# Optimization experiments

Measured on AMD Instinct MI355X. Metric: run time of the kernel, lower is better.

The kernel has to match this reference:

```python
import jax, jax.numpy as jnp
import numpy as np

NUM_HEADS = 16
HEAD_DIM = 128
MODEL_DIM = 2048
SEQ = 4096
INIT = 0.02


def setup_inputs() -> dict:
    key = jax.random.key(0)
    k1, k2, k3 = jax.random.split(key, 3)
    x = jax.random.normal(k1, (SEQ, MODEL_DIM), dtype=jnp.float32)
    w_attn = jax.random.normal(k2, (MODEL_DIM, 3 * MODEL_DIM), dtype=jnp.float32) * INIT
    b_attn = jnp.zeros((3 * MODEL_DIM,), dtype=jnp.float32)
    w_proj = jax.random.normal(k3, (MODEL_DIM, MODEL_DIM), dtype=jnp.float32) * INIT
    b_proj = jnp.zeros((MODEL_DIM,), dtype=jnp.float32)
    return {"x": x, "w_attn": w_attn, "b_attn": b_attn, "w_proj": w_proj, "b_proj": b_proj}


def reference(x, w_attn, b_attn, w_proj, b_proj):
    seq = x.shape[0]
    # fused QKV projection: [seq, 3*model_dim]
    hidden = x @ w_attn + b_attn
    q, k, v = jnp.split(hidden, 3, axis=-1)
    q = q.reshape(seq, NUM_HEADS, HEAD_DIM)
    k = k.reshape(seq, NUM_HEADS, HEAD_DIM)
    v = v.reshape(seq, NUM_HEADS, HEAD_DIM)
    q = q / jnp.sqrt(jnp.asarray(HEAD_DIM, dtype=q.dtype))
    # scores: [heads, q, k]
    scores = jnp.einsum('qhd,khd->hqk', q, k)
    causal = jnp.tril(jnp.ones((seq, seq), dtype=bool))  # mask[q, k]
    big_neg = jnp.finfo(jnp.float32).min
    scores = jnp.where(causal[None, :, :], scores, big_neg)
    pattern = jax.nn.softmax(scores, axis=-1)
    z = jnp.einsum('hqk,khd->qhd', pattern, v)
    out = z.reshape(seq, MODEL_DIM) @ w_proj + b_proj
    return out
```

## Files before the change

### kernel.cpp

```cpp
#include <hip/hip_runtime.h>
#include <hip/hip_bf16.h>
#include <stdint.h>
#include <stddef.h>

typedef __bf16 bf16_8 __attribute__((ext_vector_type(8)));
typedef __bf16 bf16_4 __attribute__((ext_vector_type(4)));
typedef float f32x4 __attribute__((ext_vector_type(4)));

#define BIG_NEG (-1e30f)
#define QSCALE (0.08838834764831845f * 1.4426950408889634f)
#define FIXMAX 16.0f

__device__ __forceinline__ void gld_lds16(const void* g, void* l) {
  __builtin_amdgcn_global_load_lds(
      (const __attribute__((address_space(1))) uint32_t*)g,
      (__attribute__((address_space(3))) uint32_t*)l, 16, 0, 0);
}

__global__ __launch_bounds__(256) void convert_bf16(
    const float* __restrict__ in, __bf16* __restrict__ out, long long n) {
  long long i = ((long long)blockIdx.x * 256 + threadIdx.x) * 8;
  if (i + 8 > n) return;
  const float4* in4 = (const float4*)(in + i);
  float4 a = in4[0], b = in4[1];
  bf16_8 o = {(__bf16)a.x, (__bf16)a.y, (__bf16)a.z, (__bf16)a.w,
              (__bf16)b.x, (__bf16)b.y, (__bf16)b.z, (__bf16)b.w};
  *(bf16_8*)(out + i) = o;
}

__global__ __launch_bounds__(256) void transpose_cvt(
    const float* __restrict__ in, __bf16* __restrict__ out, int R, int C) {
  __shared__ __bf16 tile[32][33];
  int bx = blockIdx.x * 32;
  int by = blockIdx.y * 32;
  int tx = threadIdx.x;
  int ty = threadIdx.y;
#pragma unroll
  for (int j = 0; j < 32; j += 8)
    tile[ty + j][tx] = (__bf16)in[(size_t)(by + ty + j) * C + bx + tx];
  __syncthreads();
#pragma unroll
  for (int j = 0; j < 32; j += 8)
    out[(size_t)(bx + ty + j) * R + by + tx] = tile[tx][ty + j];
}

__global__ __launch_bounds__(256) void gemm_bt(
    const __bf16* __restrict__ A, const __bf16* __restrict__ Bt,
    const float* __restrict__ bias, __bf16* __restrict__ C0,
    __bf16* __restrict__ VT, float* __restrict__ Cf,
    int M, int N, int K, int mode) {
  __shared__ __bf16 As[128 * 32];
  __shared__ __bf16 Bs[128 * 32];

  const int t = threadIdx.x;
  const int lane = t & 63;
  const int wave = t >> 6;
  const int col = lane & 15;
  const int quad = lane >> 4;
  const int wm = (wave >> 1) * 64;
  const int wn = (wave & 1) * 64;
  const int m0 = blockIdx.y * 128;
  const int n0 = blockIdx.x * 128;
  const bool vswap = (mode == 1) && (n0 >= 4096);

  const int srow = t >> 2;
  const int scol = (t & 3) * 8;
  const __bf16* ga0 = A + (size_t)(m0 + srow) * K + scol;
  const __bf16* ga1 = ga0 + (size_t)64 * K;
  const __bf16* gb0 = Bt + (size_t)(n0 + srow) * K + scol;
  const __bf16* gb1 = gb0 + (size_t)64 * K;
  __bf16* lA0 = As + wave * 512;
  __bf16* lA1 = As + 2048 + wave * 512;
  __bf16* lB0 = Bs + wave * 512;
  __bf16* lB1 = Bs + 2048 + wave * 512;

  f32x4 acc[4][4];
#pragma unroll
  for (int i = 0; i < 4; i++)
#pragma unroll
    for (int j = 0; j < 4; j++) acc[i][j] = f32x4{0.f, 0.f, 0.f, 0.f};

  for (int k0 = 0; k0 < K; k0 += 32) {
    __syncthreads();
    gld_lds16(ga0 + k0, lA0);
    gld_lds16(ga1 + k0, lA1);
    gld_lds16(gb0 + k0, lB0);
    gld_lds16(gb1 + k0, lB1);
    __syncthreads();

    bf16_8 af[4], bfr[4];
#pragma unroll
    for (int i = 0; i < 4; i++) {
      af[i] = *(const bf16_8*)(As + (wm + i * 16 + col) * 32 + quad * 8);
      bfr[i] = *(const bf16_8*)(Bs + (wn + i * 16 + col) * 32 + quad * 8);
    }
    if (!vswap) {
#pragma unroll
      for (int mi = 0; mi < 4; mi++)
#pragma unroll
        for (int ni = 0; ni < 4; ni++)
          acc[mi][ni] = __builtin_amdgcn_mfma_f32_16x16x32_bf16(
              af[mi], bfr[ni], acc[mi][ni], 0, 0, 0);
    } else {
#pragma unroll
      for (int mi = 0; mi < 4; mi++)
#pragma unroll
        for (int ni = 0; ni < 4; ni++)
          acc[mi][ni] = __builtin_amdgcn_mfma_f32_16x16x32_bf16(
              bfr[ni], af[mi], acc[mi][ni], 0, 0, 0);
    }
  }

  if (mode == 0) {
#pragma unroll
    for (int mi = 0; mi < 4; mi++)
#pragma unroll
      for (int ni = 0; ni < 4; ni++) {
        int gn = n0 + wn + ni * 16 + col;
        float bv = bias[gn];
#pragma unroll
        for (int r = 0; r < 4; r++)
          Cf[(size_t)(m0 + wm + mi * 16 + quad * 4 + r) * N + gn] =
              acc[mi][ni][r] + bv;
      }
  } else if (n0 < 2048) {
#pragma unroll
    for (int mi = 0; mi < 4; mi++)
#pragma unroll
      for (int ni = 0; ni < 4; ni++) {
        int gn = n0 + wn + ni * 16 + col;
        float bv = bias[gn];
#pragma unroll
        for (int r = 0; r < 4; r++)
          C0[(size_t)(m0 + wm + mi * 16 + quad * 4 + r) * 4096 + gn] =
              (__bf16)((acc[mi][ni][r] + bv) * QSCALE);
      }
  } else if (n0 < 4096) {
#pragma unroll
    for (int mi = 0; mi < 4; mi++)
#pragma unroll
      for (int ni = 0; ni < 4; ni++) {
        int gn = n0 + wn + ni * 16 + col;
        float bv = bias[gn];
#pragma unroll
        for (int r = 0; r < 4; r++)
          C0[(size_t)(m0 + wm + mi * 16 + quad * 4 + r) * 4096 + gn] =
              (__bf16)(acc[mi][ni][r] + bv);
      }
  } else {
#pragma unroll
    for (int mi = 0; mi < 4; mi++) {
      int seq = m0 + wm + mi * 16 + col;
#pragma unroll
      for (int ni = 0; ni < 4; ni++) {
#pragma unroll
        for (int r = 0; r < 4; r++) {
          int gn = n0 + wn + ni * 16 + quad * 4 + r;
          float bv = bias[gn];
          VT[(size_t)(gn - 4096) * M + seq] = (__bf16)(acc[mi][ni][r] + bv);
        }
      }
    }
  }
}

__global__ __launch_bounds__(256, 2) void flash_attn(
    const __bf16* __restrict__ QK, const __bf16* __restrict__ VT,
    __bf16* __restrict__ Z) {
  constexpr int KS = 136;
  constexpr int VS = 68;
  constexpr int PS = 72;
  __shared__ __bf16 Ks[64 * KS];
  __shared__ __bf16 Vs[128 * VS];
  __shared__ __bf16 Ps[2 * 4 * 16 * PS];

  const int t = threadIdx.x;
  const int lane = t & 63;
  const int wave = t >> 6;
  const int col = lane & 15;
  const int quad = lane >> 4;
  const int h = blockIdx.y;
  const int a = blockIdx.x;
  const int q0_lo = a * 64;
  const int q0_hi = (63 - a) * 64;
  const int nkb = 64 - a;

  const __bf16* kbase =
      QK + (size_t)(t >> 4) * 4096 + 2048 + h * 128 + (t & 15) * 8;
  __bf16* kdst = Ks + (t >> 4) * KS + (t & 15) * 8;
  const __bf16* vbase = VT + (size_t)(h * 128 + (t >> 3)) * 4096 + (t & 7) * 8;
  __bf16* vdst = Vs + (t >> 3) * VS + (t & 7) * 8;

  bf16_8 qf_hi[4], qf_lo[4];
  {
    const __bf16* qh = QK + (size_t)(q0_hi + wave * 16 + col) * 4096 + h * 128;
    const __bf16* ql = QK + (size_t)(q0_lo + wave * 16 + col) * 4096 + h * 128;
#pragma unroll
    for (int i = 0; i < 4; i++) {
      qf_hi[i] = *(const bf16_8*)(qh + i * 32 + quad * 8);
      qf_lo[i] = *(const bf16_8*)(ql + i * 32 + quad * 8);
    }
  }

  f32x4 z_hi[8], z_lo[8];
#pragma unroll
  for (int i = 0; i < 8; i++) {
    z_hi[i] = f32x4{0.f, 0.f, 0.f, 0.f};
    z_lo[i] = f32x4{0.f, 0.f, 0.f, 0.f};
  }
  float l_hi = 0.f, l_lo = 0.f;

  bf16_8 kpre[4], vpre[4];
#pragma unroll
  for (int j = 0; j < 4; j++) {
    kpre[j] = *(const bf16_8*)(kbase + (size_t)j * 16 * 4096);
    vpre[j] = *(const bf16_8*)(vbase + (size_t)j * 32 * 4096);
  }

  __bf16* pwh = Ps + wave * 16 * PS;
  __bf16* pwl = Ps + (4 + wave) * 16 * PS;

  for (int kb = 0; kb < nkb; kb++) {
    const int k0 = kb * 64;
    const bool lo_on = (kb <= a);
    __syncthreads();
#pragma unroll
    for (int j = 0; j < 4; j++) {
      *(bf16_8*)(kdst + j * 16 * KS) = kpre[j];
      *(bf16_8*)(vdst + j * 32 * VS) = vpre[j];
    }
    __syncthreads();

    if (kb + 1 < nkb) {
      const __bf16* kb2 = kbase + (size_t)(k0 + 64) * 4096;
      const __bf16* vb2 = vbase + (k0 + 64);
#pragma unroll
      for (int j = 0; j < 4; j++) {
        kpre[j] = *(const bf16_8*)(kb2 + (size_t)j * 16 * 4096);
        vpre[j] = *(const bf16_8*)(vb2 + (size_t)j * 32 * 4096);
      }
    }

    f32x4 sh[4], sl[4];
#pragma unroll
    for (int p = 0; p < 4; p++) {
      sh[p] = f32x4{0.f, 0.f, 0.f, 0.f};
      sl[p] = f32x4{0.f, 0.f, 0.f, 0.f};
#pragma unroll
      for (int kd = 0; kd < 4; kd++) {
        bf16_8 kf =
            *(const bf16_8*)(Ks + (p * 16 + col) * KS + kd * 32 + quad * 8);
        sh[p] =
            __builtin_amdgcn_mfma_f32_16x16x32_bf16(kf, qf_hi[kd], sh[p], 0, 0, 0);
        if (lo_on)
          sl[p] = __builtin_amdgcn_mfma_f32_16x16x32_bf16(kf, qf_lo[kd], sl[p],
                                                          0, 0, 0);
      }
    }

    if (kb == nkb - 1) {
      int qg = q0_hi + wave * 16 + col;
#pragma unroll
      for (int p = 0; p < 4; p++)
#pragma unroll
        for (int r = 0; r < 4; r++)
          if (k0 + p * 16 + quad * 4 + r > qg) sh[p][r] = BIG_NEG;
    }
    if (kb == a) {
      int qg = q0_lo + wave * 16 + col;
#pragma unroll
      for (int p = 0; p < 4; p++)
#pragma unroll
        for (int r = 0; r < 4; r++)
          if (k0 + p * 16 + quad * 4 + r > qg) sl[p][r] = BIG_NEG;
    }

    {
      float rs = 0.f;
#pragma unroll
      for (int p = 0; p < 4; p++) {
        float e0 = exp2f(sh[p][0] - FIXMAX);
        float e1 = exp2f(sh[p][1] - FIXMAX);
        float e2 = exp2f(sh[p][2] - FIXMAX);
        float e3 = exp2f(sh[p][3] - FIXMAX);
        rs += (e0 + e1) + (e2 + e3);
        bf16_4 pk = {(__bf16)e0, (__bf16)e1, (__bf16)e2, (__bf16)e3};
        *(bf16_4*)(pwh + col * PS + p * 16 + quad * 4) = pk;
      }
      l_hi += rs;
    }
    if (lo_on) {
      float rs = 0.f;
#pragma unroll
      for (int p = 0; p < 4; p++) {
        float e0 = exp2f(sl[p][0] - FIXMAX);
        float e1 = exp2f(sl[p][1] - FIXMAX);
        float e2 = exp2f(sl[p][2] - FIXMAX);
        float e3 = exp2f(sl[p][3] - FIXMAX);
        rs += (e0 + e1) + (e2 + e3);
        bf16_4 pk = {(__bf16)e0, (__bf16)e1, (__bf16)e2, (__bf16)e3};
        *(bf16_4*)(pwl + col * PS + p * 16 + quad * 4) = pk;
      }
      l_lo += rs;
    }

    bf16_8 ph0 = *(const bf16_8*)(pwh + col * PS + quad * 8);
    bf16_8 ph1 = *(const bf16_8*)(pwh + col * PS + 32 + quad * 8);
    bf16_8 pl0, pl1;
    if (lo_on) {
      pl0 = *(const bf16_8*)(pwl + col * PS + quad * 8);
      pl1 = *(const bf16_8*)(pwl + col * PS + 32 + quad * 8);
    }

#pragma unroll
    for (int db = 0; db < 8; db++) {
      bf16_8 vf0 = *(const bf16_8*)(Vs + (db * 16 + col) * VS + quad * 8);
      z_hi[db] =
          __builtin_amdgcn_mfma_f32_16x16x32_bf16(vf0, ph0, z_hi[db], 0, 0, 0);
      if (lo_on)
        z_lo[db] =
            __builtin_amdgcn_mfma_f32_16x16x32_bf16(vf0, pl0, z_lo[db], 0, 0, 0);
      bf16_8 vf1 = *(const bf16_8*)(Vs + (db * 16 + col) * VS + 32 + quad * 8);
      z_hi[db] =
          __builtin_amdgcn_mfma_f32_16x16x32_bf16(vf1, ph1, z_hi[db], 0, 0, 0);
      if (lo_on)
        z_lo[db] =
            __builtin_amdgcn_mfma_f32_16x16x32_bf16(vf1, pl1, z_lo[db], 0, 0, 0);
    }
  }

  {
    float l = l_hi;
    l += __shfl_xor(l, 16, 64);
    l += __shfl_xor(l, 32, 64);
    float rl = 1.f / l;
    __bf16* zrow =
        Z + (size_t)(q0_hi + wave * 16 + col) * 2048 + h * 128 + quad * 4;
#pragma unroll
    for (int db = 0; db < 8; db++) {
      bf16_4 o = {(__bf16)(z_hi[db][0] * rl), (__bf16)(z_hi[db][1] * rl),
                  (__bf16)(z_hi[db][2] * rl), (__bf16)(z_hi[db][3] * rl)};
      *(bf16_4*)(zrow + db * 16) = o;
    }
  }
  {
    float l = l_lo;
    l += __shfl_xor(l, 16, 64);
    l += __shfl_xor(l, 32, 64);
    float rl = 1.f / l;
    __bf16* zrow =
        Z + (size_t)(q0_lo + wave * 16 + col) * 2048 + h * 128 + quad * 4;
#pragma unroll
    for (int db = 0; db < 8; db++) {
      bf16_4 o = {(__bf16)(z_lo[db][0] * rl), (__bf16)(z_lo[db][1] * rl),
                  (__bf16)(z_lo[db][2] * rl), (__bf16)(z_lo[db][3] * rl)};
      *(bf16_4*)(zrow + db * 16) = o;
    }
  }
}

extern "C" void kernel_launch(void* const* d_in, const int* in_sizes, int n_in,
                              void* d_out, int out_size, void* d_ws,
                              size_t ws_size, hipStream_t stream) {
  const float* x = (const float*)d_in[0];
  const float* w_attn = (const float*)d_in[1];
  const float* b_attn = (const float*)d_in[2];
  const float* w_proj = (const float*)d_in[3];
  const float* b_proj = (const float*)d_in[4];
  float* out = (float*)d_out;

  __bf16* ws = (__bf16*)d_ws;
  __bf16* QK = ws;
  __bf16* VT = ws + 16777216;
  __bf16* WT1 = ws + 25165824;
  __bf16* Zb = ws + 25165824;
  __bf16* WT2 = ws + 37748736;
  __bf16* xb = ws + 41943040;

  convert_bf16<<<4096, 256, 0, stream>>>(x, xb, 8388608LL);
  transpose_cvt<<<dim3(6144 / 32, 2048 / 32), dim3(32, 8), 0, stream>>>(
      w_attn, WT1, 2048, 6144);
  transpose_cvt<<<dim3(2048 / 32, 2048 / 32), dim3(32, 8), 0, stream>>>(
      w_proj, WT2, 2048, 2048);

  gemm_bt<<<dim3(6144 / 128, 4096 / 128), 256, 0, stream>>>(
      xb, WT1, b_attn, QK, VT, nullptr, 4096, 6144, 2048, 1);

  flash_attn<<<dim3(32, 16), 256, 0, stream>>>(QK, VT, Zb);

  gemm_bt<<<dim3(2048 / 128, 4096 / 128), 256, 0, stream>>>(
      Zb, WT2, b_proj, nullptr, nullptr, out, 4096, 2048, 2048, 0);
}
```

Before: 576.5 us.

## Triple-buffer GEMM LDS tiles with async global-to-LDS prefetch

Replaces the single-buffered K loop of the bf16 GEMM with a three-stage LDS ring. Loads for tile kt+2 are issued before computing tile kt, and a partial vmcnt wait plus one barrier per iteration replaces the two syncthreads. This hides global load latency behind MFMA work. LDS use triples to 48KB per block, which can lower occupancy, and the hand-written waitcnt logic adds a risk of ordering errors.

```diff
diff --git a/kernel.cpp b/kernel.cpp
--- a/kernel.cpp
+++ b/kernel.cpp
@@ -49,8 +49,8 @@
     const float* __restrict__ bias, __bf16* __restrict__ C0,
     __bf16* __restrict__ VT, float* __restrict__ Cf,
     int M, int N, int K, int mode) {
-  __shared__ __bf16 As[128 * 32];
-  __shared__ __bf16 Bs[128 * 32];
+  __shared__ __bf16 As[3][128 * 32];
+  __shared__ __bf16 Bs[3][128 * 32];
 
   const int t = threadIdx.x;
   const int lane = t & 63;
@@ -69,10 +69,7 @@
   const __bf16* ga1 = ga0 + (size_t)64 * K;
   const __bf16* gb0 = Bt + (size_t)(n0 + srow) * K + scol;
   const __bf16* gb1 = gb0 + (size_t)64 * K;
-  __bf16* lA0 = As + wave * 512;
-  __bf16* lA1 = As + 2048 + wave * 512;
-  __bf16* lB0 = Bs + wave * 512;
-  __bf16* lB1 = Bs + 2048 + wave * 512;
+  const int ldo = wave * 512;
 
   f32x4 acc[4][4];
 #pragma unroll
@@ -80,19 +77,31 @@
 #pragma unroll
     for (int j = 0; j < 4; j++) acc[i][j] = f32x4{0.f, 0.f, 0.f, 0.f};
 
-  for (int k0 = 0; k0 < K; k0 += 32) {
-    __syncthreads();
-    gld_lds16(ga0 + k0, lA0);
-    gld_lds16(ga1 + k0, lA1);
-    gld_lds16(gb0 + k0, lB0);
-    gld_lds16(gb1 + k0, lB1);
-    __syncthreads();
+  const int nk = K / 32;
+
+#define STAGE(b, k0)                          \
+  do {                                        \
+    gld_lds16(ga0 + (k0), As[b] + ldo);       \
+    gld_lds16(ga1 + (k0), As[b] + 2048 + ldo);\
+    gld_lds16(gb0 + (k0), Bs[b] + ldo);       \
+    gld_lds16(gb1 + (k0), Bs[b] + 2048 + ldo);\
+  } while (0)
+
+  STAGE(0, 0);
+  STAGE(1, 32);
+  asm volatile("s_waitcnt vmcnt(4)" ::: "memory");
+  __builtin_amdgcn_s_barrier();
+  asm volatile("" ::: "memory");
+
+  for (int kt = 0; kt < nk; ++kt) {
+    const int b = kt % 3;
+    if (kt + 2 < nk) STAGE((kt + 2) % 3, (kt + 2) * 32);
 
     bf16_8 af[4], bfr[4];
 #pragma unroll
     for (int i = 0; i < 4; i++) {
-      af[i] = *(const bf16_8*)(As + (wm + i * 16 + col) * 32 + quad * 8);
-      bfr[i] = *(const bf16_8*)(Bs + (wn + i * 16 + col) * 32 + quad * 8);
+      af[i] = *(const bf16_8*)(As[b] + (wm + i * 16 + col) * 32 + quad * 8);
+      bfr[i] = *(const bf16_8*)(Bs[b] + (wn + i * 16 + col) * 32 + quad * 8);
     }
     if (!vswap) {
 #pragma unroll
@@ -109,7 +118,17 @@
           acc[mi][ni] = __builtin_amdgcn_mfma_f32_16x16x32_bf16(
               bfr[ni], af[mi], acc[mi][ni], 0, 0, 0);
     }
-  }
+
+    if (kt + 1 < nk) {
+      if (kt + 2 < nk)
+        asm volatile("s_waitcnt vmcnt(4)" ::: "memory");
+      else
+        asm volatile("s_waitcnt vmcnt(0)" ::: "memory");
+      __builtin_amdgcn_s_barrier();
+      asm volatile("" ::: "memory");
+    }
+  }
+#undef STAGE
 
   if (mode == 0) {
 #pragma unroll
```

New measurement: 584.3 us. No clear change (+1.4%).

## Rewrite GEMM as 256x256 tile, double-buffered, swizzled LDS with interleaved loads

Applied to the files above, without the earlier changes.

Replaces the 128x128 single-buffered GEMM with a 512-thread, 256x256-tile kernel using a K-step of 64. Shared memory is double buffered, and LDS rows are XOR-swizzled to avoid bank conflicts. Global-to-LDS loads for the tile two steps ahead are interleaved with MFMA clusters, using explicit waitcnt, barriers and priority hints. The aim is to raise data reuse and overlap memory traffic with compute. In exchange it uses 128KB of LDS and more accumulator registers, and the projection GEMM launches only 128 blocks, which may underfill the GPU.

```diff
diff --git a/kernel.cpp b/kernel.cpp
--- a/kernel.cpp
+++ b/kernel.cpp
@@ -16,6 +16,13 @@
       (const __attribute__((address_space(1))) uint32_t*)g,
       (__attribute__((address_space(3))) uint32_t*)l, 16, 0, 0);
 }
+
+#define BAR()                      \
+  do {                             \
+    asm volatile("" ::: "memory"); \
+    __builtin_amdgcn_s_barrier();  \
+    asm volatile("" ::: "memory"); \
+  } while (0)
 
 __global__ __launch_bounds__(256) void convert_bf16(
     const float* __restrict__ in, __bf16* __restrict__ out, long long n) {
@@ -44,118 +51,181 @@
     out[(size_t)(bx + ty + j) * R + by + tx] = tile[tx][ty + j];
 }
 
-__global__ __launch_bounds__(256) void gemm_bt(
+__global__ __launch_bounds__(512) void gemm_bt256(
     const __bf16* __restrict__ A, const __bf16* __restrict__ Bt,
     const float* __restrict__ bias, __bf16* __restrict__ C0,
     __bf16* __restrict__ VT, float* __restrict__ Cf,
     int M, int N, int K, int mode) {
-  __shared__ __bf16 As[128 * 32];
-  __shared__ __bf16 Bs[128 * 32];
+  __shared__ __bf16 As[2][256 * 64];
+  __shared__ __bf16 Bs[2][256 * 64];
 
   const int t = threadIdx.x;
   const int lane = t & 63;
   const int wave = t >> 6;
   const int col = lane & 15;
   const int quad = lane >> 4;
-  const int wm = (wave >> 1) * 64;
-  const int wn = (wave & 1) * 64;
-  const int m0 = blockIdx.y * 128;
-  const int n0 = blockIdx.x * 128;
+  const int wr = wave >> 2;
+  const int wc = wave & 3;
+  const int m0 = blockIdx.y * 256;
+  const int n0 = blockIdx.x * 256;
   const bool vswap = (mode == 1) && (n0 >= 4096);
 
-  const int srow = t >> 2;
-  const int scol = (t & 3) * 8;
-  const __bf16* ga0 = A + (size_t)(m0 + srow) * K + scol;
-  const __bf16* ga1 = ga0 + (size_t)64 * K;
-  const __bf16* gb0 = Bt + (size_t)(n0 + srow) * K + scol;
-  const __bf16* gb1 = gb0 + (size_t)64 * K;
-  __bf16* lA0 = As + wave * 512;
-  __bf16* lA1 = As + 2048 + wave * 512;
-  __bf16* lB0 = Bs + wave * 512;
-  __bf16* lB1 = Bs + 2048 + wave * 512;
-
-  f32x4 acc[4][4];
-#pragma unroll
-  for (int i = 0; i < 4; i++)
+  const int trow = t >> 3;
+  const int sk = (((trow & 7) ^ (t & 7)) * 8);
+  const __bf16* gA = A + (size_t)(m0 + trow) * K + sk;
+  const __bf16* gB = Bt + (size_t)(n0 + trow) * K + sk;
+  const int ldst = wave * 512;
+
+  const int ar = wr * 128 + col;
+  const int br = wc * 64 + col;
+  const int sq0 = ((quad) ^ (col & 7)) * 8;
+  const int sq1 = ((quad ^ 4) ^ (col & 7)) * 8;
+
+  f32x4 acc[8][4];
+#pragma unroll
+  for (int i = 0; i < 8; i++)
 #pragma unroll
     for (int j = 0; j < 4; j++) acc[i][j] = f32x4{0.f, 0.f, 0.f, 0.f};
 
-  for (int k0 = 0; k0 < K; k0 += 32) {
-    __syncthreads();
-    gld_lds16(ga0 + k0, lA0);
-    gld_lds16(ga1 + k0, lA1);
-    gld_lds16(gb0 + k0, lB0);
-    gld_lds16(gb1 + k0, lB1);
-    __syncthreads();
-
-    bf16_8 af[4], bfr[4];
-#pragma unroll
-    for (int i = 0; i < 4; i++) {
-      af[i] = *(const bf16_8*)(As + (wm + i * 16 + col) * 32 + quad * 8);
-      bfr[i] = *(const bf16_8*)(Bs + (wn + i * 16 + col) * 32 + quad * 8);
-    }
-    if (!vswap) {
-#pragma unroll
-      for (int mi = 0; mi < 4; mi++)
-#pragma unroll
-        for (int ni = 0; ni < 4; ni++)
-          acc[mi][ni] = __builtin_amdgcn_mfma_f32_16x16x32_bf16(
-              af[mi], bfr[ni], acc[mi][ni], 0, 0, 0);
-    } else {
-#pragma unroll
-      for (int mi = 0; mi < 4; mi++)
-#pragma unroll
-        for (int ni = 0; ni < 4; ni++)
-          acc[mi][ni] = __builtin_amdgcn_mfma_f32_16x16x32_bf16(
-              bfr[ni], af[mi], acc[mi][ni], 0, 0, 0);
-    }
-  }
+  const int nk = K / 64;
+
+#define STA(b, L, kk) \
+  gld_lds16(gA + (size_t)(L) * 64 * K + (kk), &As[b][(L) * 4096 + ldst])
+#define STB(b, L, kk) \
+  gld_lds16(gB + (size_t)(L) * 64 * K + (kk), &Bs[b][(L) * 4096 + ldst])
+
+#define CL(c)                                                              \
+  do {                                                                     \
+    if (!vswap) {                                                          \
+      _Pragma("unroll") for (int ni = 0; ni < 4; ++ni) {                   \
+        acc[2 * (c)][ni] = __builtin_amdgcn_mfma_f32_16x16x32_bf16(        \
+            af[2 * (c)][0], bfr[ni][0], acc[2 * (c)][ni], 0, 0, 0);        \
+        acc[2 * (c)][ni] = __builtin_amdgcn_mfma_f32_16x16x32_bf16(        \
+            af[2 * (c)][1], bfr[ni][1], acc[2 * (c)][ni], 0, 0, 0);        \
+        acc[2 * (c) + 1][ni] = __builtin_amdgcn_mfma_f32_16x16x32_bf16(    \
+            af[2 * (c) + 1][0], bfr[ni][0], acc[2 * (c) + 1][ni], 0, 0, 0);\
+        acc[2 * (c) + 1][ni] = __builtin_amdgcn_mfma_f32_16x16x32_bf16(    \
+            af[2 * (c) + 1][1], bfr[ni][1], acc[2 * (c) + 1][ni], 0, 0, 0);\
+      }                                                                    \
+    } else {                                                               \
+      _Pragma("unroll") for (int ni = 0; ni < 4; ++ni) {                   \
+        acc[2 * (c)][ni] = __builtin_amdgcn_mfma_f32_16x16x32_bf16(        \
+            bfr[ni][0], af[2 * (c)][0], acc[2 * (c)][ni], 0, 0, 0);        \
+        acc[2 * (c)][ni] = __builtin_amdgcn_mfma_f32_16x16x32_bf16(        \
+            bfr[ni][1], af[2 * (c)][1], acc[2 * (c)][ni], 0, 0, 0);        \
+        acc[2 * (c) + 1][ni] = __builtin_amdgcn_mfma_f32_16x16x32_bf16(    \
+            bfr[ni][0], af[2 * (c) + 1][0], acc[2 * (c) + 1][ni], 0, 0, 0);\
+        acc[2 * (c) + 1][ni] = __builtin_amdgcn_mfma_f32_16x16x32_bf16(    \
+            bfr[ni][1], af[2 * (c) + 1][1], acc[2 * (c) + 1][ni], 0, 0, 0);\
+      }                                                                    \
+    }                                                                      \
+  } while (0)
+
+  STA(0, 0, 0); STA(0, 1, 0); STA(0, 2, 0); STA(0, 3, 0);
+  STB(0, 0, 0); STB(0, 1, 0); STB(0, 2, 0); STB(0, 3, 0);
+  STA(1, 0, 64); STA(1, 1, 64); STA(1, 2, 64); STA(1, 3, 64);
+  STB(1, 0, 64); STB(1, 1, 64); STB(1, 2, 64); STB(1, 3, 64);
+  asm volatile("s_waitcnt vmcnt(8)" ::: "memory");
+  BAR();
+
+  for (int kt = 0; kt < nk; ++kt) {
+    const int cb = kt & 1;
+    const int kk = (kt + 2) * 64;
+    const bool st = (kt + 2) < nk;
+
+    bf16_8 af[8][2], bfr[4][2];
+#pragma unroll
+    for (int mi = 0; mi < 4; ++mi) {
+      af[mi][0] = *(const bf16_8*)(&As[cb][(ar + mi * 16) * 64 + sq0]);
+      af[mi][1] = *(const bf16_8*)(&As[cb][(ar + mi * 16) * 64 + sq1]);
+    }
+#pragma unroll
+    for (int ni = 0; ni < 4; ++ni) {
+      bfr[ni][0] = *(const bf16_8*)(&Bs[cb][(br + ni * 16) * 64 + sq0]);
+      bfr[ni][1] = *(const bf16_8*)(&Bs[cb][(br + ni * 16) * 64 + sq1]);
+    }
+    asm volatile("s_waitcnt lgkmcnt(0)" ::: "memory");
+    __builtin_amdgcn_sched_barrier(0);
+    __builtin_amdgcn_s_setprio(1);
+    CL(0);
+    __builtin_amdgcn_s_setprio(0);
+
+#pragma unroll
+    for (int mi = 4; mi < 8; ++mi) {
+      af[mi][0] = *(const bf16_8*)(&As[cb][(ar + mi * 16) * 64 + sq0]);
+      af[mi][1] = *(const bf16_8*)(&As[cb][(ar + mi * 16) * 64 + sq1]);
+    }
+    BAR();
+    if (st) { STB(cb, 0, kk); STB(cb, 1, kk); STB(cb, 2, kk); STB(cb, 3, kk); }
+    asm volatile("s_waitcnt lgkmcnt(0)" ::: "memory");
+    __builtin_amdgcn_sched_barrier(0);
+    __builtin_amdgcn_s_setprio(1);
+    CL(1);
+    __builtin_amdgcn_s_setprio(0);
+
+    BAR();
+    if (st) { STA(cb, 0, kk); STA(cb, 1, kk); }
+    __builtin_amdgcn_s_setprio(1);
+    CL(2);
+    __builtin_amdgcn_s_setprio(0);
+    if (st) { STA(cb, 2, kk); STA(cb, 3, kk); }
+    __builtin_amdgcn_s_setprio(1);
+    CL(3);
+    __builtin_amdgcn_s_setprio(0);
+    if (st)
+      asm volatile("s_waitcnt vmcnt(8)" ::: "memory");
+    else
+      asm volatile("s_waitcnt vmcnt(0)" ::: "memory");
+    BAR();
+  }
+#undef STA
+#undef STB
 
   if (mode == 0) {
 #pragma unroll
-    for (int mi = 0; mi < 4; mi++)
+    for (int mi = 0; mi < 8; mi++)
 #pragma unroll
       for (int ni = 0; ni < 4; ni++) {
-        int gn = n0 + wn + ni * 16 + col;
+        int gn = n0 + wc * 64 + ni * 16 + col;
         float bv = bias[gn];
 #pragma unroll
         for (int r = 0; r < 4; r++)
-          Cf[(size_t)(m0 + wm + mi * 16 + quad * 4 + r) * N + gn] =
+          Cf[(size_t)(m0 + wr * 128 + mi * 16 + quad * 4 + r) * N + gn] =
               acc[mi][ni][r] + bv;
       }
   } else if (n0 < 2048) {
 #pragma unroll
-    for (int mi = 0; mi < 4; mi++)
+    for (int mi = 0; mi < 8; mi++)
 #pragma unroll
       for (int ni = 0; ni < 4; ni++) {
-        int gn = n0 + wn + ni * 16 + col;
+        int gn = n0 + wc * 64 + ni * 16 + col;
         float bv = bias[gn];
 #pragma unroll
         for (int r = 0; r < 4; r++)
-          C0[(size_t)(m0 + wm + mi * 16 + quad * 4 + r) * 4096 + gn] =
+          C0[(size_t)(m0 + wr * 128 + mi * 16 + quad * 4 + r) * 4096 + gn] =
               (__bf16)((acc[mi][ni][r] + bv) * QSCALE);
       }
   } else if (n0 < 4096) {
 #pragma unroll
-    for (int mi = 0; mi < 4; mi++)
+    for (int mi = 0; mi < 8; mi++)
 #pragma unroll
       for (int ni = 0; ni < 4; ni++) {
-        int gn = n0 + wn + ni * 16 + col;
+        int gn = n0 + wc * 64 + ni * 16 + col;
         float bv = bias[gn];
 #pragma unroll
         for (int r = 0; r < 4; r++)
-          C0[(size_t)(m0 + wm + mi * 16 + quad * 4 + r) * 4096 + gn] =
+          C0[(size_t)(m0 + wr * 128 + mi * 16 + quad * 4 + r) * 4096 + gn] =
               (__bf16)(acc[mi][ni][r] + bv);
       }
   } else {
 #pragma unroll
-    for (int mi = 0; mi < 4; mi++) {
-      int seq = m0 + wm + mi * 16 + col;
+    for (int mi = 0; mi < 8; mi++) {
+      int seq = m0 + wr * 128 + mi * 16 + col;
 #pragma unroll
       for (int ni = 0; ni < 4; ni++) {
 #pragma unroll
         for (int r = 0; r < 4; r++) {
-          int gn = n0 + wn + ni * 16 + quad * 4 + r;
+          int gn = n0 + wc * 64 + ni * 16 + quad * 4 + r;
           float bv = bias[gn];
           VT[(size_t)(gn - 4096) * M + seq] = (__bf16)(acc[mi][ni][r] + bv);
         }
@@ -383,11 +453,11 @@
   transpose_cvt<<<dim3(2048 / 32, 2048 / 32), dim3(32, 8), 0, stream>>>(
       w_proj, WT2, 2048, 2048);
 
-  gemm_bt<<<dim3(6144 / 128, 4096 / 128), 256, 0, stream>>>(
+  gemm_bt256<<<dim3(6144 / 256, 4096 / 256), 512, 0, stream>>>(
       xb, WT1, b_attn, QK, VT, nullptr, 4096, 6144, 2048, 1);
 
   flash_attn<<<dim3(32, 16), 256, 0, stream>>>(QK, VT, Zb);
 
-  gemm_bt<<<dim3(2048 / 128, 4096 / 128), 256, 0, stream>>>(
+  gemm_bt256<<<dim3(2048 / 256, 4096 / 256), 512, 0, stream>>>(
       Zb, WT2, b_proj, nullptr, nullptr, out, 4096, 2048, 2048, 0);
 }
```

Result: slower. 829.9 us (+44.0%).
